# Kernel tuning notes

Hardware: AMD Instinct MI355X
Metric: run time of the kernel (lower is better)

## Reference

```python
import jax, jax.numpy as jnp
import numpy as np

N, C_IN, C_OUT, T, V = 128, 64, 64, 128, 25
GROUPS, K = 8, 3
REL = C_IN // 8  # rel_reduction=8, in_channels>16


def setup_inputs() -> dict:
    key = jax.random.key(0)
    ks = jax.random.split(key, 16)
    f = lambda k, sh, s=0.05: (jax.random.normal(k, sh) * s).astype(jnp.float32)
    return {
        "x0": jax.random.normal(ks[0], (N, C_IN, T, V), jnp.float32),
        "DecoupleA": f(ks[1], (K, GROUPS, V, V), 0.2),
        "A": f(ks[2], (K, V, V), 0.2),
        "alpha": jnp.full((1,), 0.5, jnp.float32),
        "w1": f(ks[3], (K, REL, C_IN)), "b1": f(ks[4], (K, REL)),
        "w2": f(ks[5], (K, REL, C_IN)), "b2": f(ks[6], (K, REL)),
        "w3": f(ks[7], (K, C_OUT, C_IN)), "b3": f(ks[8], (K, C_OUT)),
        "w4": f(ks[9], (K, C_OUT, REL)), "b4": f(ks[10], (K, C_OUT)),
        "Linear_weight": f(ks[11], (C_IN, C_OUT * K)),
        "Linear_bias": f(ks[12], (1, C_OUT * K, 1, 1)),
        "bn0_gamma": jnp.ones((C_OUT * K,), jnp.float32),
        "bn0_beta": jnp.zeros((C_OUT * K,), jnp.float32),
        "ens_w": f(ks[13], (C_OUT, 2 * C_OUT)), "ens_b": f(ks[14], (C_OUT,)),
        "bn_gamma": jnp.full((C_OUT,), 1e-6, jnp.float32),
        "bn_beta": jnp.zeros((C_OUT,), jnp.float32),
    }


def _bn(x, gamma, beta, eps=1e-5):
    # training-mode BatchNorm2d over NCHW: stats over (N, T, V)
    mu = x.mean(axis=(0, 2, 3), keepdims=True)
    var = x.var(axis=(0, 2, 3), keepdims=True)
    return (x - mu) * jax.lax.rsqrt(var + eps) * gamma[None, :, None, None] + beta[None, :, None, None]


def _norm_adj(A):
    # torch: D = A.sum(dim=rows) -> column sums; A @ diag(1/(D+1e-3)) scales columns
    d = A.sum(axis=-2)  # [..., V] column sums
    return A * (1.0 / (d + 0.001))[..., None, :]


def reference(x0, DecoupleA, A, alpha, w1, b1, w2, b2, w3, b3, w4, b4,
              Linear_weight, Linear_bias, bn0_gamma, bn0_beta, ens_w, ens_b,
              bn_gamma, bn_beta):
    n, c_in, t, v = x0.shape
    k, g = DecoupleA.shape[0], DecoupleA.shape[1]
    c_out = w3.shape[1]
    # DecoupleA.repeat(1, out_channels//groups, 1, 1) == tile along channel dim
    learn_A = jnp.tile(DecoupleA, (1, c_out // g, 1, 1))  # [K, C_OUT, V, V]
    norm_A = _norm_adj(learn_A)
    # decoupled linear path
    x = jnp.einsum('nctv,cd->ndtv', x0, Linear_weight) + Linear_bias
    x = _bn(x, bn0_gamma, bn0_beta)
    x = x.reshape(n, k, c_out, t, v)
    x = jnp.einsum('nkctv,kcvw->nctw', x, norm_A)  # [n, C_OUT, t, v]
    # CTRGC branches (conv-then-mean over T == mean-then-1x1 since conv is linear)
    xm = x0.mean(axis=2)  # [n, c_in, v]
    y = jnp.zeros((n, c_out, t, v), x0.dtype)
    for i in range(k):
        x1 = jnp.einsum('ncv,rc->nrv', xm, w1[i]) + b1[i][:, None]
        x2 = jnp.einsum('ncv,rc->nrv', xm, w2[i]) + b2[i][:, None]
        diff = jnp.tanh(x1[:, :, :, None] - x2[:, :, None, :])        # [n, rel, u, w]
        att = jnp.einsum('nruw,or->nouw', diff, w4[i]) + b4[i][None, :, None, None]
        att = att * alpha[0] + A[i][None, None]                        # [n, C_OUT, u, w]
        x3 = jnp.einsum('nctv,oc->notv', x0, w3[i]) + b3[i][None, :, None, None]
        y = y + jnp.einsum('ncuv,nctu->nctv', att, x3)
    cat = jnp.concatenate([x, y], axis=1)                              # [n, 2*C_OUT, t, v]
    out = jnp.einsum('nctv,oc->notv', cat, ens_w) + ens_b[None, :, None, None]
    out = _bn(out, bn_gamma, bn_beta)
    out = out + x0  # down is identity since in_channels == out_channels
    return jax.nn.relu(out)
```

## Files before the change

### kernel.cpp

```cpp
#include <hip/hip_runtime.h>
#include <cstddef>
#include <cstring>

typedef _Float16 h8 __attribute__((ext_vector_type(8)));
typedef _Float16 h4v __attribute__((ext_vector_type(4)));
typedef float f4 __attribute__((ext_vector_type(4)));
typedef unsigned int u32;
typedef unsigned short u16;

#define MTOT 409600.0f

#define DO_XM  15360000
#define DO_GP  15564800
#define DO_GR  16613376

#define WS_OB16 0
#define WS_ATT  13631488
#define WS_ATTB 23461888
#define WS_BN2P 23666688
#define WS_PAR  23827456
#define WS_CSN  23828000

#define ATT_H 27262976
#define NAB_H 47595520
#define CB_H  47620096
#define WA_H  47622144
#define W3_H  47634432
#define EW_H  47646720

#define LDS_DYN 116736

__global__ __launch_bounds__(512) void k_gram(const float* __restrict__ x0,
                                              float* __restrict__ gp) {
  __shared__ _Float16 Xs[64 * 128];
  char* smb = (char*)Xs;
  int bid = blockIdx.x, tid = threadIdx.x;
  int n = bid >> 1, sh = bid & 1;
  int base = sh * 1536;
  int niter = sh ? 13 : 12;
  const float* xb = x0 + (size_t)n * 204800;
  int wid = tid >> 6, lane = tid & 63, l15 = lane & 15, l4 = lane >> 4;
  int ca = (wid & 3) * 16;
  int jb0 = (wid >> 2) * 2;
  f4 acc[2] = {{0.f, 0.f, 0.f, 0.f}, {0.f, 0.f, 0.f, 0.f}};
  int sc = tid >> 3, scol = (tid & 7) * 16;
  int swz = (sc & 7) << 4;
  for (int it = 0; it < niter; ++it) {
    int s0 = base + it * 128;
    __syncthreads();
    const float* src = xb + sc * 3200 + s0 + scol;
#pragma unroll
    for (int j = 0; j < 4; ++j) {
      float4 f = *(const float4*)(src + j * 4);
      h4v hv = {(_Float16)f.x, (_Float16)f.y, (_Float16)f.z, (_Float16)f.w};
      *(h4v*)(smb + sc * 256 + (((scol + j * 4) * 2) ^ swz)) = hv;
    }
    __syncthreads();
#pragma unroll
    for (int kk = 0; kk < 4; ++kk) {
      int kb = kk * 64 + l4 * 16;
      int arow = ca + l15;
      h8 af = *(const h8*)(smb + arow * 256 + (kb ^ ((arow & 7) << 4)));
#pragma unroll
      for (int j = 0; j < 2; ++j) {
        int brow = (jb0 + j) * 16 + l15;
        h8 bf = *(const h8*)(smb + brow * 256 + (kb ^ ((brow & 7) << 4)));
        acc[j] = __builtin_amdgcn_mfma_f32_16x16x32_f16(af, bf, acc[j], 0, 0, 0);
      }
    }
  }
  float* o = gp + (size_t)bid * 4096;
#pragma unroll
  for (int j = 0; j < 2; ++j)
#pragma unroll
    for (int q = 0; q < 4; ++q)
      o[(ca + l4 * 4 + q) * 64 + (jb0 + j) * 16 + l15] = acc[j][q];
}

__global__ __launch_bounds__(256) void k_gred(float* __restrict__ dsc) {
  int bid = blockIdx.x, tid = threadIdx.x;
  if (bid < 16) {
    int idx = bid * 256 + tid;
    const float* gp = dsc + DO_GP;
    float s0 = 0.f, s1 = 0.f, s2 = 0.f, s3 = 0.f;
    for (int b = 0; b < 256; b += 4) {
      s0 += gp[(size_t)b * 4096 + idx];
      s1 += gp[(size_t)(b + 1) * 4096 + idx];
      s2 += gp[(size_t)(b + 2) * 4096 + idx];
      s3 += gp[(size_t)(b + 3) * 4096 + idx];
    }
    dsc[DO_GR + idx] = (s0 + s1) + (s2 + s3);
  } else {
    __shared__ float red[64][5];
    int c = tid >> 2, j = tid & 3;
    float s = 0.f;
    for (int nn = j; nn < 128; nn += 4) {
      const float* xmp = dsc + DO_XM + (size_t)(nn * 64 + c) * 25;
      for (int v = 0; v < 25; ++v) s += xmp[v];
    }
    red[c][j] = s;
    __syncthreads();
    if (j == 0)
      dsc[DO_GR + 4096 + c] = 128.f * (red[c][0] + red[c][1] + red[c][2] + red[c][3]);
  }
}

__global__ __launch_bounds__(256) void k_xm(const float* __restrict__ x0,
                                            float* __restrict__ dsc,
                                            float* __restrict__ ws) {
  __shared__ float red[8][32];
  int bid = blockIdx.x;
  int gid = bid * 256 + threadIdx.x;
  if (gid < 204800) ws[WS_ATTB + gid] = 0.f;
  int n = bid >> 6, c = bid & 63;
  int tid = threadIdx.x;
  int tq = tid >> 5, v = tid & 31;
  const float* xb = x0 + (size_t)(n * 64 + c) * 3200;
  float s = 0.f;
  if (v < 25) {
    for (int j = 0; j < 16; j++) s += xb[(tq + 8 * j) * 25 + v];
  }
  red[tq][v] = s;
  __syncthreads();
  if (tq == 0 && v < 25) {
    float tot = 0.f;
#pragma unroll
    for (int q = 0; q < 8; q++) tot += red[q][v];
    dsc[DO_XM + (size_t)(n * 64 + c) * 25 + v] = tot * (1.0f / 128.0f);
  }
}

__global__ __launch_bounds__(256) void k_prep(const float* __restrict__ DA,
                                              const float* __restrict__ w3,
                                              const float* __restrict__ ensw,
                                              float* __restrict__ wsF) {
  int bid = blockIdx.x, tid = threadIdx.x;
  _Float16* wsH = (_Float16*)wsF;
  if (bid < 3) {
    if (tid < 200) {
      int k = bid, g = tid / 25, w = tid % 25;
      const float* base = DA + (k * 8 + g) * 625 + w;
      float s = 0.f;
      for (int v = 0; v < 25; v++) s += base[v * 25];
      float inv = 1.0f / (s + 0.001f);
      wsF[WS_CSN + k * 200 + g * 25 + w] = s * inv;
      _Float16* dst = wsH + NAB_H + (size_t)((k * 8 + g) * 32 + w) * 32;
      for (int v = 0; v < 25; v++) dst[v] = (_Float16)(base[v * 25] * inv);
      for (int v = 25; v < 32; v++) dst[v] = (_Float16)0.f;
    }
  } else if (bid == 3) {
    for (int idx = tid; idx < 5376; idx += 256) {
      int kg = idx / 224, r = idx % 224;
      int w = 25 + r / 32, v = r & 31;
      wsH[NAB_H + (size_t)(kg * 32 + w) * 32 + v] = (_Float16)0.f;
    }
  } else if (bid < 12) {
    int i0 = (bid - 4) * 1536;
    for (int i = tid; i < 1536; i += 256)
      wsH[W3_H + i0 + i] = (_Float16)w3[i0 + i];
  } else {
    int i0 = (bid - 12) * 2048;
    for (int i = tid; i < 2048; i += 256)
      wsH[EW_H + i0 + i] = (_Float16)ensw[i0 + i];
  }
}

__global__ __launch_bounds__(256) void k_bnstat(const float* __restrict__ dsc,
                                                const float* __restrict__ Lw,
                                                const float* __restrict__ g0,
                                                const float* __restrict__ b0,
                                                float* __restrict__ wsF) {
  __shared__ float Gsh[64 * 66];
  __shared__ float Ly[64][17];
  __shared__ float part[16][17];
  __shared__ float a1L[16];
  int bid = blockIdx.x, tid = threadIdx.x;
  int d0 = bid * 16, dl = tid >> 4, r = tid & 15, d = d0 + dl;
  for (int idx = tid; idx < 4096; idx += 256)
    Gsh[(idx >> 6) * 66 + (idx & 63)] = dsc[DO_GR + idx];
  for (int idx = tid; idx < 1024; idx += 256)
    Ly[idx >> 4][idx & 15] = Lw[(idx >> 4) * 192 + d0 + (idx & 15)];
  __syncthreads();
  float acc = 0.f;
#pragma unroll
  for (int cc = 0; cc < 4; ++cc) {
    int c = r * 4 + cc;
    float h = 0.f;
    for (int c2 = 0; c2 < 64; ++c2) h += Gsh[c * 66 + c2] * Ly[c2][dl];
    acc += Ly[c][dl] * h;
  }
  part[dl][r] = acc;
  __syncthreads();
  if (r == 0) {
    float ex2 = 0.f;
#pragma unroll
    for (int i = 0; i < 16; ++i) ex2 += part[dl][i];
    ex2 *= (1.0f / MTOT);
    float mu = 0.f;
    for (int c = 0; c < 64; ++c) mu += dsc[DO_GR + 4096 + c] * Ly[c][dl];
    mu *= (1.0f / MTOT);
    float var = ex2 - mu * mu;
    float a1 = g0[d] * rsqrtf(var + 1e-5f);
    float b1c = b0[d] - a1 * mu;
    wsF[WS_PAR + 128 + d] = a1;
    wsF[WS_PAR + 320 + d] = b1c;
    a1L[dl] = a1;
  }
  __syncthreads();
  _Float16* wsH = (_Float16*)wsF;
  int k = d >> 6, cg = d & 63;
  float a1v = a1L[dl];
#pragma unroll
  for (int j = 0; j < 4; ++j) {
    int e = r * 4 + j;
    wsH[WA_H + k * 4096 + cg * 64 + e] = (_Float16)(a1v * Lw[e * 192 + d]);
  }
}

__global__ __launch_bounds__(256) void k_cb(float* __restrict__ wsF) {
  int tid = threadIdx.x;
  _Float16* wsH = (_Float16*)wsF;
  for (int idx = tid; idx < 2048; idx += 256) {
    int c = idx >> 5, w = idx & 31;
    float s = 0.f;
    if (w < 25) {
      int g = c & 7;
      for (int k = 0; k < 3; ++k)
        s += wsF[WS_PAR + 320 + k * 64 + c] * wsF[WS_CSN + k * 200 + g * 25 + w];
    }
    wsH[CB_H + idx] = (_Float16)s;
  }
}

__global__ __launch_bounds__(256) void k_att(const float* __restrict__ dsc,
    const float* __restrict__ w1, const float* __restrict__ b1,
    const float* __restrict__ w2, const float* __restrict__ b2,
    const float* __restrict__ w4, const float* __restrict__ b4,
    const float* __restrict__ Ag, const float* __restrict__ alpha,
    const float* __restrict__ b3, float* __restrict__ wsF) {
  __shared__ float xms[1600];
  __shared__ float x1s[200];
  __shared__ float x2s[200];
  __shared__ float Td[5000];
  int bid = blockIdx.x, tid = threadIdx.x;
  int n = bid / 3, i = bid % 3;
  for (int idx = tid; idx < 1600; idx += 256)
    xms[idx] = dsc[DO_XM + (size_t)n * 1600 + idx];
  __syncthreads();
  for (int idx = tid; idx < 400; idx += 256) {
    int r = (idx % 200) / 25, u = idx % 25;
    const float* wv = (idx < 200 ? w1 : w2) + (i * 8 + r) * 64;
    float acc = (idx < 200 ? b1 : b2)[i * 8 + r];
    for (int c = 0; c < 64; c++) acc += xms[c * 25 + u] * wv[c];
    if (idx < 200) x1s[r * 25 + u] = acc; else x2s[r * 25 + u] = acc;
  }
  __syncthreads();
  for (int idx = tid; idx < 5000; idx += 256) {
    int r = idx / 625, u = (idx % 625) / 25, w = idx % 25;
    Td[idx] = tanhf(x1s[r * 25 + u] - x2s[r * 25 + w]);
  }
  __syncthreads();
  float al = alpha[0];
  u32* attW = (u32*)wsF;
  for (int p = tid; p < 1600; p += 256) {
    int o = p / 25, w = p % 25;
    float w4r[8];
#pragma unroll
    for (int r = 0; r < 8; r++) w4r[r] = w4[(i * 64 + o) * 8 + r];
    float b4v = b4[i * 64 + o];
    const float* AgW = Ag + i * 625 + w;
    float asum = 0.f;
    size_t rowH = (size_t)ATT_H + ((size_t)((n * 3 + i) * 64 + o) * 25 + w) * 32;
    u32* row = attW + rowH / 2;
    for (int up = 0; up < 16; ++up) {
      u32 word = 0;
#pragma unroll
      for (int h = 0; h < 2; ++h) {
        int u = up * 2 + h;
        float v = 0.f;
        if (u < 25) {
          float acc = b4v;
#pragma unroll
          for (int r = 0; r < 8; r++) acc += w4r[r] * Td[r * 625 + u * 25 + w];
          v = al * acc + AgW[u * 25];
          asum += v;
        }
        union { _Float16 hf; u16 b; } cv;
        cv.hf = (_Float16)v;
        word |= ((u32)cv.b) << (16 * h);
      }
      row[up] = word;
    }
    atomicAdd(&wsF[WS_ATTB + (size_t)n * 1600 + p], b3[i * 64 + o] * asum);
  }
}

__device__ __forceinline__ void stageX(const float* __restrict__ xn, char* sm, int tid) {
  for (int u = tid; u < 6400; u += 1024) {
    int cg = u / 400, s = u - cg * 400;
    int c0 = cg * 4;
    const float* p = xn + c0 * 3200 + s;
    float a = p[0], b = p[3200], c = p[6400], d = p[9600];
    h4v hv = {(_Float16)a, (_Float16)b, (_Float16)c, (_Float16)d};
    *(h4v*)(sm + s * 128 + ((c0 * 2) ^ ((s & 7) << 4))) = hv;
  }
}
__device__ __forceinline__ void zeroHpads(char* sm, int tid) {
  for (int idx = tid; idx < 7168; idx += 1024) {
    int c = idx / 112, r = idx % 112;
    int t = r / 7, u = 25 + r % 7;
    int hs = (((t & 3) ^ ((c >> 2) & 3)) << 4);
    *(_Float16*)(sm + 51200 + c * 1024 + t * 64 + ((u * 2) ^ hs)) = (_Float16)0.f;
  }
}
__device__ __forceinline__ void gemm64(const _Float16* __restrict__ Aw, char* sm,
                                       int mt, int nt0, int nt1, int lane) {
  int l15 = lane & 15, l4 = lane >> 4;
  h8 a0 = *(const h8*)(Aw + (mt * 16 + l15) * 64 + l4 * 8);
  h8 a1 = *(const h8*)(Aw + (mt * 16 + l15) * 64 + 32 + l4 * 8);
  for (int nt = nt0; nt < nt1; ++nt) {
    int s = nt * 16 + l15;
    int sw = (s & 7) << 4;
    const char* rb = sm + s * 128;
    h8 b0 = *(const h8*)(rb + ((l4 * 16) ^ sw));
    h8 b1 = *(const h8*)(rb + ((64 + l4 * 16) ^ sw));
    f4 acc = {0.f, 0.f, 0.f, 0.f};
    acc = __builtin_amdgcn_mfma_f32_16x16x32_f16(a0, b0, acc, 0, 0, 0);
    acc = __builtin_amdgcn_mfma_f32_16x16x32_f16(a1, b1, acc, 0, 0, 0);
    int t = s / 25, u = s % 25;
#pragma unroll
    for (int q = 0; q < 4; ++q) {
      int c = mt * 16 + l4 * 4 + q;
      int hs = (((t & 3) ^ ((c >> 2) & 3)) << 4);
      *(_Float16*)(sm + 51200 + c * 1024 + t * 64 + ((u * 2) ^ hs)) = (_Float16)acc[q];
    }
  }
}

__global__ __launch_bounds__(1024, 4) void kAB(const float* __restrict__ x0,
                                               float* ws,
                                               const float* __restrict__ ensb) {
  extern __shared__ char sm[];
  __shared__ float redS[128];
  __shared__ float attBs[1600];
  const _Float16* wsH = (const _Float16*)ws;
  int tid = threadIdx.x, bid = blockIdx.x;
  int lb = (bid & 7) * 128 + (bid >> 3);
  int n = lb >> 3, tile = lb & 7;
  int wid = tid >> 6, lane = tid & 63, l15 = lane & 15, l4 = lane >> 4;
  int mt = wid & 3, q4 = wid >> 2, g = wid & 7;
  int nt0 = q4 ? 1 + 6 * q4 : 0;
  int nt1 = q4 ? nt0 + 6 : 7;
  if (tid < 128) redS[tid] = 0.f;
  for (int idx = tid; idx < 1600; idx += 1024)
    attBs[idx] = ws[WS_ATTB + (size_t)n * 1600 + idx];
  stageX(x0 + (size_t)n * 204800 + tile * 400, sm, tid);
  zeroHpads(sm, tid);
  __syncthreads();
  f4 accx[4][2], accy[4][2];
#pragma unroll
  for (int a = 0; a < 4; a++)
#pragma unroll
    for (int b = 0; b < 2; b++) {
      accx[a][b] = (f4){0.f, 0.f, 0.f, 0.f};
      accy[a][b] = (f4){0.f, 0.f, 0.f, 0.f};
    }
  for (int k = 0; k < 3; ++k) {
    gemm64(wsH + WA_H + k * 4096, sm, mt, nt0, nt1, lane);
    __syncthreads();
#pragma unroll
    for (int mt2 = 0; mt2 < 4; ++mt2) {
      int c = mt2 * 16 + wid;
      int hs = (((l15 & 3) ^ ((c >> 2) & 3)) << 4);
      h8 aH = *(const h8*)(sm + 51200 + c * 1024 + l15 * 64 + ((l4 * 16) ^ hs));
#pragma unroll
      for (int nt2 = 0; nt2 < 2; ++nt2) {
        const _Float16* nb = wsH + NAB_H +
            (size_t)((k * 8 + g) * 32 + nt2 * 16 + l15) * 32 + l4 * 8;
        accx[mt2][nt2] = __builtin_amdgcn_mfma_f32_16x16x32_f16(
            aH, *(const h8*)nb, accx[mt2][nt2], 0, 0, 0);
      }
    }
    __syncthreads();
  }
  for (int i = 0; i < 3; ++i) {
    gemm64(wsH + W3_H + i * 4096, sm, mt, nt0, nt1, lane);
    __syncthreads();
#pragma unroll
    for (int mt2 = 0; mt2 < 4; ++mt2) {
      int c = mt2 * 16 + wid;
      int hs = (((l15 & 3) ^ ((c >> 2) & 3)) << 4);
      h8 aX = *(const h8*)(sm + 51200 + c * 1024 + l15 * 64 + ((l4 * 16) ^ hs));
#pragma unroll
      for (int nt2 = 0; nt2 < 2; ++nt2) {
        int v = nt2 * 16 + l15;
        int vc = v < 25 ? v : 0;
        const _Float16* ab = wsH + ATT_H +
            ((size_t)((n * 3 + i) * 64 + c) * 25 + vc) * 32 + l4 * 8;
        accy[mt2][nt2] = __builtin_amdgcn_mfma_f32_16x16x32_f16(
            aX, *(const h8*)ab, accy[mt2][nt2], 0, 0, 0);
      }
    }
    __syncthreads();
  }
#pragma unroll
  for (int mt2 = 0; mt2 < 4; ++mt2) {
    int c = mt2 * 16 + wid;
#pragma unroll
    for (int nt2 = 0; nt2 < 2; ++nt2) {
      int w = nt2 * 16 + l15;
      if (w < 25) {
        float cbv = (float)wsH[CB_H + c * 32 + w];
        float abv = attBs[c * 25 + w];
#pragma unroll
        for (int q = 0; q < 4; ++q) {
          int t = l4 * 4 + q;
          int s = t * 25 + w;
          int sw = (s & 7) << 4;
          *(_Float16*)(sm + s * 256 + ((c * 2) ^ sw)) =
              (_Float16)(accx[mt2][nt2][q] + cbv);
          *(_Float16*)(sm + s * 256 + (((64 + c) * 2) ^ sw)) =
              (_Float16)(accy[mt2][nt2][q] + abv);
        }
      }
    }
  }
  __syncthreads();
  h8 ea[4];
#pragma unroll
  for (int ks = 0; ks < 4; ++ks)
    ea[ks] = *(const h8*)(wsH + EW_H + (mt * 16 + l15) * 128 + ks * 32 + l4 * 8);
  float eb[4];
#pragma unroll
  for (int q = 0; q < 4; ++q) eb[q] = ensb[mt * 16 + l4 * 4 + q];
  float lsum[4] = {0.f, 0.f, 0.f, 0.f}, lss[4] = {0.f, 0.f, 0.f, 0.f};
  u16* ob16 = (u16*)ws;
  for (int nt = nt0; nt < nt1; ++nt) {
    int s = nt * 16 + l15;
    int sw = (s & 7) << 4;
    f4 acc = {0.f, 0.f, 0.f, 0.f};
#pragma unroll
    for (int ks = 0; ks < 4; ++ks) {
      h8 b = *(const h8*)(sm + s * 256 + (((ks * 32 + l4 * 8) * 2) ^ sw));
      acc = __builtin_amdgcn_mfma_f32_16x16x32_f16(ea[ks], b, acc, 0, 0, 0);
    }
    size_t ob = (size_t)n * 204800 + (size_t)tile * 400 + s;
#pragma unroll
    for (int q = 0; q < 4; ++q) {
      int o = mt * 16 + l4 * 4 + q;
      union { _Float16 hf; u16 b; } cv;
      cv.hf = (_Float16)(acc[q] + eb[q]);
      ob16[ob + (size_t)o * 3200] = cv.b;
      float val = (float)cv.hf;
      lsum[q] += val;
      lss[q] += val * val;
    }
  }
#pragma unroll
  for (int q = 0; q < 4; ++q) {
#pragma unroll
    for (int d = 1; d < 16; d <<= 1) {
      lsum[q] += __shfl_xor(lsum[q], d);
      lss[q] += __shfl_xor(lss[q], d);
    }
  }
  if (l15 == 0) {
#pragma unroll
    for (int q = 0; q < 4; ++q) {
      int o = mt * 16 + l4 * 4 + q;
      atomicAdd(&redS[o], lsum[q]);
      atomicAdd(&redS[64 + o], lss[q]);
    }
  }
  __syncthreads();
  if (tid < 64) {
    ws[WS_BN2P + (size_t)bid * 128 + tid * 2] = redS[tid];
    ws[WS_BN2P + (size_t)bid * 128 + tid * 2 + 1] = redS[64 + tid];
  }
}

__global__ __launch_bounds__(256) void k_bn2(const float* __restrict__ g2,
                                             const float* __restrict__ b2,
                                             float* __restrict__ ws) {
  __shared__ float rs[256], rss[256];
  int o = blockIdx.x, tid = threadIdx.x;
  float s = 0.f, ss = 0.f;
  for (int b = tid; b < 1024; b += 256) {
    s += ws[WS_BN2P + (size_t)b * 128 + o * 2];
    ss += ws[WS_BN2P + (size_t)b * 128 + o * 2 + 1];
  }
  rs[tid] = s; rss[tid] = ss;
  __syncthreads();
  for (int st = 128; st > 0; st >>= 1) {
    if (tid < st) { rs[tid] += rs[tid + st]; rss[tid] += rss[tid + st]; }
    __syncthreads();
  }
  if (tid == 0) {
    float mu = rs[0] / MTOT;
    float var = rss[0] / MTOT - mu * mu;
    float a2 = g2[o] * rsqrtf(var + 1e-5f);
    ws[WS_PAR + o] = a2;
    ws[WS_PAR + 64 + o] = b2[o] - a2 * mu;
  }
}

__global__ __launch_bounds__(256) void k_final(const float* __restrict__ x0,
                                               const float* __restrict__ ws,
                                               float* __restrict__ dout) {
  size_t g = (size_t)blockIdx.x * 256 + threadIdx.x;
  h4v p = reinterpret_cast<const h4v*>(ws)[g];
  float4 x = reinterpret_cast<const float4*>(x0)[g];
  int o = (int)((g * 4 / 3200) & 63);
  float a2 = ws[WS_PAR + o], bc = ws[WS_PAR + 64 + o];
  float4 r;
  r.x = fmaxf(fmaf(a2, (float)p[0], bc) + x.x, 0.f);
  r.y = fmaxf(fmaf(a2, (float)p[1], bc) + x.y, 0.f);
  r.z = fmaxf(fmaf(a2, (float)p[2], bc) + x.z, 0.f);
  r.w = fmaxf(fmaf(a2, (float)p[3], bc) + x.w, 0.f);
  reinterpret_cast<float4*>(dout)[g] = r;
}

extern "C" void kernel_launch(void* const* d_in, const int* in_sizes, int n_in,
                              void* d_out, int out_size, void* d_ws, size_t ws_size,
                              hipStream_t stream) {
  const float* x0    = (const float*)d_in[0];
  const float* DA    = (const float*)d_in[1];
  const float* Ag    = (const float*)d_in[2];
  const float* alpha = (const float*)d_in[3];
  const float* w1    = (const float*)d_in[4];
  const float* b1    = (const float*)d_in[5];
  const float* w2    = (const float*)d_in[6];
  const float* b2    = (const float*)d_in[7];
  const float* w3    = (const float*)d_in[8];
  const float* b3    = (const float*)d_in[9];
  const float* w4    = (const float*)d_in[10];
  const float* b4    = (const float*)d_in[11];
  const float* Lw    = (const float*)d_in[12];
  const float* g0    = (const float*)d_in[14];
  const float* b0    = (const float*)d_in[15];
  const float* ensw  = (const float*)d_in[16];
  const float* ensb  = (const float*)d_in[17];
  const float* g2    = (const float*)d_in[18];
  const float* b2n   = (const float*)d_in[19];
  float* out = (float*)d_out;
  float* ws  = (float*)d_ws;

  hipFuncSetAttribute((const void*)kAB, hipFuncAttributeMaxDynamicSharedMemorySize, LDS_DYN);

  k_xm<<<8192, 256, 0, stream>>>(x0, out, ws);
  k_gram<<<256, 512, 0, stream>>>(x0, out + DO_GP);
  k_prep<<<16, 256, 0, stream>>>(DA, w3, ensw, ws);
  k_att<<<384, 256, 0, stream>>>(out, w1, b1, w2, b2, w4, b4, Ag, alpha, b3, ws);
  k_gred<<<17, 256, 0, stream>>>(out);
  k_bnstat<<<12, 256, 0, stream>>>(out, Lw, g0, b0, ws);
  k_cb<<<1, 256, 0, stream>>>(ws);
  kAB<<<1024, 1024, LDS_DYN, stream>>>(x0, ws, ensb);
  k_bn2<<<64, 256, 0, stream>>>(g2, b2n, ws);
  k_final<<<25600, 256, 0, stream>>>(x0, ws, out);
}
```

Before: 300.5 us.

## Merge prep into gram kernel, compute cb in kAB, simplify gemm64 indexing

Folds the k_prep weight-conversion work into extra blocks of k_gram and drops the single-block k_cb kernel by computing the bias table per block inside kAB into shared memory. The ATTB zeroing moves from k_xm to a hipMemsetAsync. Together these cut the launch count by one. The stageX loop now maps consecutive threads to channel groups, and gemm64 computes its store address incrementally instead of dividing per tile. The trade-off is that every kAB block recomputes the small cb table and uses more static LDS, which could affect occupancy.

```diff
diff --git a/kernel.cpp b/kernel.cpp
--- a/kernel.cpp
+++ b/kernel.cpp
@@ -23,7 +23,6 @@
 
 #define ATT_H 27262976
 #define NAB_H 47595520
-#define CB_H  47620096
 #define WA_H  47622144
 #define W3_H  47634432
 #define EW_H  47646720
@@ -31,10 +30,46 @@
 #define LDS_DYN 116736
 
 __global__ __launch_bounds__(512) void k_gram(const float* __restrict__ x0,
-                                              float* __restrict__ gp) {
+                                              float* __restrict__ gp,
+                                              const float* __restrict__ DA,
+                                              const float* __restrict__ w3,
+                                              const float* __restrict__ ensw,
+                                              float* __restrict__ wsF) {
+  int bid = blockIdx.x, tid = threadIdx.x;
+  if (bid >= 256) {
+    int pb = bid - 256;
+    _Float16* wsH = (_Float16*)wsF;
+    if (pb < 3) {
+      if (tid < 200) {
+        int k = pb, g = tid / 25, w = tid % 25;
+        const float* base = DA + (k * 8 + g) * 625 + w;
+        float s = 0.f;
+        for (int v = 0; v < 25; v++) s += base[v * 25];
+        float inv = 1.0f / (s + 0.001f);
+        wsF[WS_CSN + k * 200 + g * 25 + w] = s * inv;
+        _Float16* dst = wsH + NAB_H + (size_t)((k * 8 + g) * 32 + w) * 32;
+        for (int v = 0; v < 25; v++) dst[v] = (_Float16)(base[v * 25] * inv);
+        for (int v = 25; v < 32; v++) dst[v] = (_Float16)0.f;
+      }
+    } else if (pb == 3) {
+      for (int idx = tid; idx < 5376; idx += 512) {
+        int kg = idx / 224, r = idx % 224;
+        int w = 25 + r / 32, v = r & 31;
+        wsH[NAB_H + (size_t)(kg * 32 + w) * 32 + v] = (_Float16)0.f;
+      }
+    } else if (pb < 12) {
+      int i0 = (pb - 4) * 1536;
+      for (int i = tid; i < 1536; i += 512)
+        wsH[W3_H + i0 + i] = (_Float16)w3[i0 + i];
+    } else {
+      int i0 = (pb - 12) * 2048;
+      for (int i = tid; i < 2048; i += 512)
+        wsH[EW_H + i0 + i] = (_Float16)ensw[i0 + i];
+    }
+    return;
+  }
   __shared__ _Float16 Xs[64 * 128];
   char* smb = (char*)Xs;
-  int bid = blockIdx.x, tid = threadIdx.x;
   int n = bid >> 1, sh = bid & 1;
   int base = sh * 1536;
   int niter = sh ? 13 : 12;
@@ -106,12 +141,9 @@
 }
 
 __global__ __launch_bounds__(256) void k_xm(const float* __restrict__ x0,
-                                            float* __restrict__ dsc,
-                                            float* __restrict__ ws) {
+                                            float* __restrict__ dsc) {
   __shared__ float red[8][32];
   int bid = blockIdx.x;
-  int gid = bid * 256 + threadIdx.x;
-  if (gid < 204800) ws[WS_ATTB + gid] = 0.f;
   int n = bid >> 6, c = bid & 63;
   int tid = threadIdx.x;
   int tq = tid >> 5, v = tid & 31;
@@ -127,41 +159,6 @@
 #pragma unroll
     for (int q = 0; q < 8; q++) tot += red[q][v];
     dsc[DO_XM + (size_t)(n * 64 + c) * 25 + v] = tot * (1.0f / 128.0f);
-  }
-}
-
-__global__ __launch_bounds__(256) void k_prep(const float* __restrict__ DA,
-                                              const float* __restrict__ w3,
-                                              const float* __restrict__ ensw,
-                                              float* __restrict__ wsF) {
-  int bid = blockIdx.x, tid = threadIdx.x;
-  _Float16* wsH = (_Float16*)wsF;
-  if (bid < 3) {
-    if (tid < 200) {
-      int k = bid, g = tid / 25, w = tid % 25;
-      const float* base = DA + (k * 8 + g) * 625 + w;
-      float s = 0.f;
-      for (int v = 0; v < 25; v++) s += base[v * 25];
-      float inv = 1.0f / (s + 0.001f);
-      wsF[WS_CSN + k * 200 + g * 25 + w] = s * inv;
-      _Float16* dst = wsH + NAB_H + (size_t)((k * 8 + g) * 32 + w) * 32;
-      for (int v = 0; v < 25; v++) dst[v] = (_Float16)(base[v * 25] * inv);
-      for (int v = 25; v < 32; v++) dst[v] = (_Float16)0.f;
-    }
-  } else if (bid == 3) {
-    for (int idx = tid; idx < 5376; idx += 256) {
-      int kg = idx / 224, r = idx % 224;
-      int w = 25 + r / 32, v = r & 31;
-      wsH[NAB_H + (size_t)(kg * 32 + w) * 32 + v] = (_Float16)0.f;
-    }
-  } else if (bid < 12) {
-    int i0 = (bid - 4) * 1536;
-    for (int i = tid; i < 1536; i += 256)
-      wsH[W3_H + i0 + i] = (_Float16)w3[i0 + i];
-  } else {
-    int i0 = (bid - 12) * 2048;
-    for (int i = tid; i < 2048; i += 256)
-      wsH[EW_H + i0 + i] = (_Float16)ensw[i0 + i];
   }
 }
 
@@ -217,21 +214,6 @@
   }
 }
 
-__global__ __launch_bounds__(256) void k_cb(float* __restrict__ wsF) {
-  int tid = threadIdx.x;
-  _Float16* wsH = (_Float16*)wsF;
-  for (int idx = tid; idx < 2048; idx += 256) {
-    int c = idx >> 5, w = idx & 31;
-    float s = 0.f;
-    if (w < 25) {
-      int g = c & 7;
-      for (int k = 0; k < 3; ++k)
-        s += wsF[WS_PAR + 320 + k * 64 + c] * wsF[WS_CSN + k * 200 + g * 25 + w];
-    }
-    wsH[CB_H + idx] = (_Float16)s;
-  }
-}
-
 __global__ __launch_bounds__(256) void k_att(const float* __restrict__ dsc,
     const float* __restrict__ w1, const float* __restrict__ b1,
     const float* __restrict__ w2, const float* __restrict__ b2,
@@ -296,8 +278,8 @@
 }
 
 __device__ __forceinline__ void stageX(const float* __restrict__ xn, char* sm, int tid) {
-  for (int u = tid; u < 6400; u += 1024) {
-    int cg = u / 400, s = u - cg * 400;
+  for (int uu = tid; uu < 6400; uu += 1024) {
+    int cg = uu & 15, s = uu >> 4;
     int c0 = cg * 4;
     const float* p = xn + c0 * 3200 + s;
     float a = p[0], b = p[3200], c = p[6400], d = p[9600];
@@ -318,8 +300,10 @@
   int l15 = lane & 15, l4 = lane >> 4;
   h8 a0 = *(const h8*)(Aw + (mt * 16 + l15) * 64 + l4 * 8);
   h8 a1 = *(const h8*)(Aw + (mt * 16 + l15) * 64 + 32 + l4 * 8);
+  int s = nt0 * 16 + l15;
+  int t = s / 25, u = s - t * 25;
+  int hsc = ((mt * 4 + l4) & 3) << 4;
   for (int nt = nt0; nt < nt1; ++nt) {
-    int s = nt * 16 + l15;
     int sw = (s & 7) << 4;
     const char* rb = sm + s * 128;
     h8 b0 = *(const h8*)(rb + ((l4 * 16) ^ sw));
@@ -327,13 +311,14 @@
     f4 acc = {0.f, 0.f, 0.f, 0.f};
     acc = __builtin_amdgcn_mfma_f32_16x16x32_f16(a0, b0, acc, 0, 0, 0);
     acc = __builtin_amdgcn_mfma_f32_16x16x32_f16(a1, b1, acc, 0, 0, 0);
-    int t = s / 25, u = s % 25;
-#pragma unroll
-    for (int q = 0; q < 4; ++q) {
-      int c = mt * 16 + l4 * 4 + q;
-      int hs = (((t & 3) ^ ((c >> 2) & 3)) << 4);
-      *(_Float16*)(sm + 51200 + c * 1024 + t * 64 + ((u * 2) ^ hs)) = (_Float16)acc[q];
-    }
+    int hs = ((t & 3) << 4) ^ hsc;
+    char* wb = sm + 51200 + (mt * 16 + l4 * 4) * 1024 + t * 64 + ((u * 2) ^ hs);
+#pragma unroll
+    for (int q = 0; q < 4; ++q)
+      *(_Float16*)(wb + q * 1024) = (_Float16)acc[q];
+    s += 16;
+    u += 16;
+    if (u >= 25) { u -= 25; ++t; }
   }
 }
 
@@ -343,6 +328,7 @@
   extern __shared__ char sm[];
   __shared__ float redS[128];
   __shared__ float attBs[1600];
+  __shared__ float cbS[1600];
   const _Float16* wsH = (const _Float16*)ws;
   int tid = threadIdx.x, bid = blockIdx.x;
   int lb = (bid & 7) * 128 + (bid >> 3);
@@ -354,6 +340,15 @@
   if (tid < 128) redS[tid] = 0.f;
   for (int idx = tid; idx < 1600; idx += 1024)
     attBs[idx] = ws[WS_ATTB + (size_t)n * 1600 + idx];
+  for (int idx = tid; idx < 1600; idx += 1024) {
+    int c = idx / 25, w = idx - c * 25;
+    int gg = c & 7;
+    float s = 0.f;
+#pragma unroll
+    for (int k = 0; k < 3; ++k)
+      s += ws[WS_PAR + 320 + k * 64 + c] * ws[WS_CSN + k * 200 + gg * 25 + w];
+    cbS[idx] = s;
+  }
   stageX(x0 + (size_t)n * 204800 + tile * 400, sm, tid);
   zeroHpads(sm, tid);
   __syncthreads();
@@ -410,7 +405,7 @@
     for (int nt2 = 0; nt2 < 2; ++nt2) {
       int w = nt2 * 16 + l15;
       if (w < 25) {
-        float cbv = (float)wsH[CB_H + c * 32 + w];
+        float cbv = cbS[c * 25 + w];
         float abv = attBs[c * 25 + w];
 #pragma unroll
         for (int q = 0; q < 4; ++q) {
@@ -547,13 +542,12 @@
 
   hipFuncSetAttribute((const void*)kAB, hipFuncAttributeMaxDynamicSharedMemorySize, LDS_DYN);
 
-  k_xm<<<8192, 256, 0, stream>>>(x0, out, ws);
-  k_gram<<<256, 512, 0, stream>>>(x0, out + DO_GP);
-  k_prep<<<16, 256, 0, stream>>>(DA, w3, ensw, ws);
+  hipMemsetAsync(ws + WS_ATTB, 0, 204800 * sizeof(float), stream);
+  k_xm<<<8192, 256, 0, stream>>>(x0, out);
+  k_gram<<<272, 512, 0, stream>>>(x0, out + DO_GP, DA, w3, ensw, ws);
   k_att<<<384, 256, 0, stream>>>(out, w1, b1, w2, b2, w4, b4, Ag, alpha, b3, ws);
   k_gred<<<17, 256, 0, stream>>>(out);
   k_bnstat<<<12, 256, 0, stream>>>(out, Lw, g0, b0, ws);
-  k_cb<<<1, 256, 0, stream>>>(ws);
   kAB<<<1024, 1024, LDS_DYN, stream>>>(x0, ws, ensb);
   k_bn2<<<64, 256, 0, stream>>>(g2, b2n, ws);
   k_final<<<25600, 256, 0, stream>>>(x0, ws, out);
```

After: 320.4 us. 1.07x slower.
